# Kernel tuning notes

Hardware: AMD Instinct MI355X
Metric: run time of the kernel (lower is better)

## Reference

```python
import jax, jax.numpy as jnp
import numpy as np

G, T, D = 4, 4096, 2048      # num_groups, tokens_per_group, d_model
E, K, C = 64, 2, 128         # num_experts, num_selected_experts, expert_capacity


def setup_inputs() -> dict:
    key = jax.random.key(0)
    k1, k2 = jax.random.split(key, 2)
    token_inputs = jax.random.normal(k1, (G, T, D), dtype=jnp.float32)
    W = jax.random.normal(k2, (D, E), dtype=jnp.float32) * 0.02  # RouterWeights init std=0.02
    b = jnp.zeros((E,), dtype=jnp.float32)
    return {"token_inputs": token_inputs, "W": W, "b": b,
            "num_experts": E, "expert_capacity": C}


def _route(token_inputs, W, b, num_experts, expert_capacity, k=K, bpr=True):
    # jitter_noise = 0.0 and ignore_padding_tokens = False -> no jitter, no padding mask
    logits = jnp.einsum('gtd,de->gte', token_inputs, W) + b          # [g,t,e]
    probs = jax.nn.softmax(logits, axis=-1)                          # [g,t,e]

    expert_gate, expert_index = jax.lax.top_k(probs, k)              # [g,t,k]

    # Switch Transformer load-balancing loss (eqs 4-6)
    em_lb = jnp.max(jax.nn.one_hot(expert_index, num_experts, dtype=jnp.float32), axis=-2)  # [g,t,e]
    aux_loss = jnp.mean(jnp.mean(em_lb, axis=-2) * jnp.mean(probs, axis=-2)) * num_experts ** 2

    # Batch Prioritized Routing: sort tokens by top-1 gate, descending
    if bpr:
        perm = jnp.argsort(-expert_gate[..., 0], axis=-1)            # [g,t]
        expert_index = jnp.take_along_axis(expert_index, perm[..., None], axis=-2)

    g = token_inputs.shape[0]
    # [g,t,k] -> [g,k,t] -> [g,k*t]: all top-1 choices before top-2 choices
    ei = jnp.transpose(expert_index, (0, 2, 1)).reshape(g, -1)
    em = jax.nn.one_hot(ei, num_experts, dtype=jnp.int32)            # [g,k*t,e]
    # position of each token within its chosen expert's buffer (capacity assignment)
    token_priority = jnp.cumsum(em, axis=1) * em - 1.0               # [g,k*t,e]
    token_priority = token_priority.reshape(g, k, -1, num_experts).transpose(0, 2, 1, 3)
    token_priority = jnp.max(token_priority, axis=2)                 # [g,t,e]

    if bpr:
        inv_perm = jnp.argsort(perm, axis=-1)
        token_priority = jnp.take_along_axis(token_priority, inv_perm[..., None], axis=-2)

    # priority >= expert_capacity or < 0 -> dropped (one_hot gives all zeros)
    dispatch = jax.nn.one_hot(token_priority, expert_capacity, dtype=jnp.float32)  # [g,t,e,c]
    combine = probs[..., None] * dispatch                            # [g,t,e,c]

    z_loss = jnp.mean(jnp.square(jax.nn.log_softmax(logits, axis=-1)))
    return dispatch.astype(jnp.bool_), combine, aux_loss, z_loss


def reference(token_inputs, W, b, num_experts, expert_capacity):
    return _route(token_inputs, W, b, num_experts, expert_capacity)
```

## Files before the change

### kernel.cpp

```cpp
#include <hip/hip_runtime.h>
#include <math.h>

constexpr int Gn = 4;
constexpr int Tn = 4096;
constexpr int Dn = 2048;
constexpr int En = 64;
constexpr int Cn = 128;
constexpr int NT = Gn * Tn;
constexpr size_t NDC = (size_t)NT * En * Cn;


__global__ __launch_bounds__(1024) void k_main(
    const float* __restrict__ x, const float* __restrict__ Wm,
    const float* __restrict__ bias,
    float* __restrict__ gate, int* __restrict__ e1a, int* __restrict__ e2a,
    float* __restrict__ p1a, float* __restrict__ p2a,
    double* __restrict__ spartG, double* __restrict__ zpartArr)
{
    __shared__ float xs[64 * 68];
    __shared__ float ws[64 * 64];
    __shared__ double zrow[64];

    const int tid  = threadIdx.x;
    const int lane = tid & 63;
    const int wave = tid >> 6;
    const int er   = lane & 15;
    const int tr   = lane >> 4;
    const int row  = wave * 4 + tr;
    const int tok0 = blockIdx.x * 64;

    const int sx_row = tid >> 4;
    const int sx_col = tid & 15;

    float acc[4] = {0.f, 0.f, 0.f, 0.f};

    float4 px = *(const float4*)(x + (size_t)(tok0 + sx_row) * Dn + 4 * sx_col);
    float4 pw = ((const float4*)Wm)[tid];

    const float* xsp = xs + row * 68;
    const float* wsp = ws + 4 * er;

    for (int it = 0; it < 32; ++it) {
        *(float4*)(xs + sx_row * 68 + 4 * sx_col) = px;
        ((float4*)ws)[tid] = pw;
        __syncthreads();

        if (it < 31) {
            const int k0 = (it + 1) * 64;
            px = *(const float4*)(x + (size_t)(tok0 + sx_row) * Dn + k0 + 4 * sx_col);
            pw = ((const float4*)(Wm + (size_t)k0 * En))[tid];
        }

        {
        #pragma clang fp contract(off)
        #pragma unroll 4
        for (int kk = 0; kk < 16; ++kk) {
            float4 xq = *(const float4*)(xsp + 4 * kk);
            #pragma unroll
            for (int j = 0; j < 4; ++j) {
                float4 wf = *(const float4*)(wsp + (4 * kk + j) * 64);
                float xv = ((const float*)&xq)[j];
                acc[0] = acc[0] + xv * wf.x;
                acc[1] = acc[1] + xv * wf.y;
                acc[2] = acc[2] + xv * wf.z;
                acc[3] = acc[3] + xv * wf.w;
            }
        }
        }
        __syncthreads();
    }

    {
    #pragma clang fp contract(off)
    #pragma unroll
    for (int j = 0; j < 4; ++j)
        xs[row * 68 + 4 * er + j] = acc[j] + bias[4 * er + j];
    }
    __syncthreads();

    if (tid < 64) {
        const float* lrow = xs + tid * 68;
        float* erow = ws + tid * 64;

        float m = lrow[0];
        for (int i = 1; i < 64; ++i) m = fmaxf(m, lrow[i]);

        for (int i = 0; i < 64; ++i) {
            float d = lrow[i] - m;
            erow[i] = (float)exp((double)d);
        }

        float r8[8];
        #pragma unroll
        for (int j2 = 0; j2 < 8; ++j2) r8[j2] = erow[j2];
        for (int mIt = 1; mIt < 8; ++mIt)
            #pragma unroll
            for (int j2 = 0; j2 < 8; ++j2) r8[j2] += erow[8 * mIt + j2];
        float S = ((r8[0] + r8[1]) + (r8[2] + r8[3]))
                + ((r8[4] + r8[5]) + (r8[6] + r8[7]));

        float av = -1.0f, bv = -1.0f; int ai = 0, bi = 0;
        for (int i = 0; i < 64; ++i) {
            float p = erow[i] / S;
            erow[i] = p;
            if (p > av)      { bv = av; bi = ai; av = p; ai = i; }
            else if (p > bv) { bv = p; bi = i; }
        }

        int tok = tok0 + tid;
        gate[tok] = av;
        e1a[tok] = ai;
        e2a[tok] = bi;
        p1a[tok] = av;
        p2a[tok] = bv;

        double lse = (double)m + log((double)S);
        double zz = 0.0;
        for (int i = 0; i < 64; ++i) {
            double d = (double)lrow[i] - lse;
            zz += d * d;
        }
        zrow[tid] = zz;
    }
    __syncthreads();

    if (tid < 64) {
        double s = 0.0;
        for (int t2 = 0; t2 < 64; ++t2) s += (double)ws[t2 * 64 + tid];
        spartG[blockIdx.x * 64 + tid] = s;
        if (tid == 0) {
            double z = 0.0;
            for (int t2 = 0; t2 < 64; ++t2) z += zrow[t2];
            zpartArr[blockIdx.x] = z;
        }
    }
}

__global__ __launch_bounds__(1024) void k_sortfill(
    const float* __restrict__ gate,
    const int* __restrict__ e1a, const int* __restrict__ e2a,
    int* __restrict__ eseq, int* __restrict__ tseq)
{
    __shared__ float key[4096];
    __shared__ int   val[4096];

    const int g = blockIdx.x;
    for (int i = threadIdx.x; i < Tn; i += 1024) {
        key[i] = gate[g * Tn + i];
        val[i] = i;
    }
    __syncthreads();
    for (int k = 2; k <= Tn; k <<= 1) {
        for (int j = k >> 1; j > 0; j >>= 1) {
            for (int i = threadIdx.x; i < Tn; i += 1024) {
                int ixj = i ^ j;
                if (ixj > i) {
                    bool dir = ((i & k) == 0);
                    float ka = key[i], kb = key[ixj];
                    int   va = val[i], vb = val[ixj];
                    bool bFirst = (kb > ka) || (kb == ka && vb < va);
                    if (bFirst == dir) {
                        key[i] = kb; key[ixj] = ka;
                        val[i] = vb; val[ixj] = va;
                    }
                }
            }
            __syncthreads();
        }
    }
    for (int i = threadIdx.x; i < Tn; i += 1024) {
        int tok = val[i];
        int b = g * 2 * Tn;
        tseq[b + i]      = tok;
        tseq[b + Tn + i] = tok;
        eseq[b + i]      = e1a[g * Tn + tok];
        eseq[b + Tn + i] = e2a[g * Tn + tok];
    }
}

__global__ __launch_bounds__(256) void k_priofill(
    const int* __restrict__ eseq, const int* __restrict__ tseq,
    int* __restrict__ pr1, int* __restrict__ pr2, int* __restrict__ cnt)
{
    if (threadIdx.x >= 64) return;

    const int g = blockIdx.x;
    const int lane = threadIdx.x;
    const int gb = g * 2 * Tn;
    int base = 0;

    int e   = eseq[gb + lane];
    int tok = tseq[gb + lane];

    for (int c = 0; c < 2 * Tn / 64; ++c) {
        int en = 0, tn2 = 0;
        if (c < 2 * Tn / 64 - 1) {
            en  = eseq[gb + (c + 1) * 64 + lane];
            tn2 = tseq[gb + (c + 1) * 64 + lane];
        }

        unsigned long long m  = ~0ull;
        unsigned long long mo = ~0ull;
        #pragma unroll
        for (int bb = 0; bb < 6; ++bb) {
            unsigned long long bal = __ballot((e >> bb) & 1);
            m  &= ((e    >> bb) & 1) ? bal : ~bal;
            mo &= ((lane >> bb) & 1) ? bal : ~bal;
        }
        int rank   = __popcll(m & ((1ull << lane) - 1ull));
        int myBase = __shfl(base, e);
        int pr     = myBase + rank;
        int j      = c * 64 + lane;
        if (j < Tn) pr1[g * Tn + tok] = pr;
        else        pr2[g * Tn + tok] = pr;
        base += __popcll(mo);

        e = en; tok = tn2;
    }
    cnt[g * En + lane] = base;
}

__global__ __launch_bounds__(256) void k_scatfin(
    const int* __restrict__ e1a, const int* __restrict__ e2a,
    const float* __restrict__ p1a, const float* __restrict__ p2a,
    const int* __restrict__ pr1, const int* __restrict__ pr2,
    const int* __restrict__ cnt, const double* __restrict__ spartG,
    const double* __restrict__ zpartArr, float* __restrict__ out)
{
    if (blockIdx.x == 64) {
        __shared__ double red[256];
        __shared__ double zred[256];
        int t = threadIdx.x;
        int g = t >> 6, e = t & 63;
        double s = 0.0;
        #pragma unroll 8
        for (int lb = 0; lb < 64; ++lb)
            s += spartG[((g << 6) + lb) * 64 + e];
        red[t]  = (double)cnt[t] * s;
        zred[t] = zpartArr[t];
        __syncthreads();
        for (int st = 128; st; st >>= 1) {
            if (t < st) { red[t] += red[t + st]; zred[t] += zred[t + st]; }
            __syncthreads();
        }
        if (t == 0) {
            double aux = red[0] * ((double)En / ((double)Gn * (double)Tn * (double)Tn));
            out[2 * NDC]     = (float)aux;
            out[2 * NDC + 1] = (float)(zred[0] / ((double)Gn * Tn * En));
        }
        return;
    }

    int tok = blockIdx.x * 256 + threadIdx.x;
    size_t base = (size_t)tok * En * Cn;
    int p = pr1[tok];
    if (p < Cn) {
        size_t o = base + (size_t)e1a[tok] * Cn + p;
        out[o] = 1.0f;
        out[NDC + o] = p1a[tok];
    }
    p = pr2[tok];
    if (p < Cn) {
        size_t o = base + (size_t)e2a[tok] * Cn + p;
        out[o] = 1.0f;
        out[NDC + o] = p2a[tok];
    }
}

extern "C" void kernel_launch(void* const* d_in, const int* in_sizes, int n_in,
                              void* d_out, int out_size, void* d_ws, size_t ws_size,
                              hipStream_t stream)
{
    const float* x    = (const float*)d_in[0];
    const float* Wm   = (const float*)d_in[1];
    const float* bias = (const float*)d_in[2];
    float* out = (float*)d_out;

    double* spartG   = (double*)d_ws;
    double* zpartArr = spartG + 256 * 64;
    float* gate = (float*)(zpartArr + 256);
    float* p1a  = gate + NT;
    float* p2a  = p1a + NT;
    int* e1a  = (int*)(p2a + NT);
    int* e2a  = e1a + NT;
    int* pr1  = e2a + NT;
    int* pr2  = pr1 + NT;
    int* cnt  = pr2 + NT;
    int* eseq = cnt + Gn * En;
    int* tseq = eseq + Gn * 2 * Tn;

    k_main<<<256, 1024, 0, stream>>>(x, Wm, bias, gate, e1a, e2a,
                                     p1a, p2a, spartG, zpartArr);

    k_sortfill<<<4, 1024, 0, stream>>>(gate, e1a, e2a, eseq, tseq);

    k_priofill<<<4, 256, 0, stream>>>(eseq, tseq, pr1, pr2, cnt);

    k_scatfin<<<65, 256, 0, stream>>>(e1a, e2a, p1a, p2a, pr1, pr2,
                                      cnt, spartG, zpartArr, out);
}
```

Before: 1.151 ms.

## Replace global bitonic sort and serial priority scan with per-expert rank counting

Drops the per-group bitonic sort and the single-wave sequential priority scan. Instead it launches one block per (group, expert) that collects that expert's tokens and computes each token's capacity position by counting higher-gated tokens in the same expert. This moves the work from 4 lightly parallel blocks to 256 blocks. The cost is quadratic in tokens per expert, which is small for balanced routing but could grow with skewed routing.

Result: faster. 1.059 ms (-8.0%).

```diff
diff --git a/kernel.cpp b/kernel.cpp
--- a/kernel.cpp
+++ b/kernel.cpp
@@ -136,88 +136,64 @@
     }
 }
 
-__global__ __launch_bounds__(1024) void k_sortfill(
+__global__ __launch_bounds__(256) void k_rank(
     const float* __restrict__ gate,
     const int* __restrict__ e1a, const int* __restrict__ e2a,
-    int* __restrict__ eseq, int* __restrict__ tseq)
-{
-    __shared__ float key[4096];
-    __shared__ int   val[4096];
-
-    const int g = blockIdx.x;
-    for (int i = threadIdx.x; i < Tn; i += 1024) {
-        key[i] = gate[g * Tn + i];
-        val[i] = i;
-    }
-    __syncthreads();
-    for (int k = 2; k <= Tn; k <<= 1) {
-        for (int j = k >> 1; j > 0; j >>= 1) {
-            for (int i = threadIdx.x; i < Tn; i += 1024) {
-                int ixj = i ^ j;
-                if (ixj > i) {
-                    bool dir = ((i & k) == 0);
-                    float ka = key[i], kb = key[ixj];
-                    int   va = val[i], vb = val[ixj];
-                    bool bFirst = (kb > ka) || (kb == ka && vb < va);
-                    if (bFirst == dir) {
-                        key[i] = kb; key[ixj] = ka;
-                        val[i] = vb; val[ixj] = va;
-                    }
-                }
-            }
-            __syncthreads();
-        }
-    }
-    for (int i = threadIdx.x; i < Tn; i += 1024) {
-        int tok = val[i];
-        int b = g * 2 * Tn;
-        tseq[b + i]      = tok;
-        tseq[b + Tn + i] = tok;
-        eseq[b + i]      = e1a[g * Tn + tok];
-        eseq[b + Tn + i] = e2a[g * Tn + tok];
-    }
-}
-
-__global__ __launch_bounds__(256) void k_priofill(
-    const int* __restrict__ eseq, const int* __restrict__ tseq,
     int* __restrict__ pr1, int* __restrict__ pr2, int* __restrict__ cnt)
 {
-    if (threadIdx.x >= 64) return;
-
-    const int g = blockIdx.x;
-    const int lane = threadIdx.x;
-    const int gb = g * 2 * Tn;
-    int base = 0;
-
-    int e   = eseq[gb + lane];
-    int tok = tseq[gb + lane];
-
-    for (int c = 0; c < 2 * Tn / 64; ++c) {
-        int en = 0, tn2 = 0;
-        if (c < 2 * Tn / 64 - 1) {
-            en  = eseq[gb + (c + 1) * 64 + lane];
-            tn2 = tseq[gb + (c + 1) * 64 + lane];
-        }
-
-        unsigned long long m  = ~0ull;
-        unsigned long long mo = ~0ull;
-        #pragma unroll
-        for (int bb = 0; bb < 6; ++bb) {
-            unsigned long long bal = __ballot((e >> bb) & 1);
-            m  &= ((e    >> bb) & 1) ? bal : ~bal;
-            mo &= ((lane >> bb) & 1) ? bal : ~bal;
-        }
-        int rank   = __popcll(m & ((1ull << lane) - 1ull));
-        int myBase = __shfl(base, e);
-        int pr     = myBase + rank;
-        int j      = c * 64 + lane;
-        if (j < Tn) pr1[g * Tn + tok] = pr;
-        else        pr2[g * Tn + tok] = pr;
-        base += __popcll(mo);
-
-        e = en; tok = tn2;
-    }
-    cnt[g * En + lane] = base;
+    __shared__ int   ltok[4096];
+    __shared__ float lgat[4096];
+    __shared__ int   ncnt;
+
+    const int g = blockIdx.x >> 6;
+    const int e = blockIdx.x & 63;
+    const int tid = threadIdx.x;
+    const int gb = g * Tn;
+
+    if (tid == 0) ncnt = 0;
+    __syncthreads();
+    for (int t = tid; t < Tn; t += 256) {
+        if (e1a[gb + t] == e) {
+            int idx = atomicAdd(&ncnt, 1);
+            ltok[idx] = t;
+            lgat[idx] = gate[gb + t];
+        }
+    }
+    __syncthreads();
+    const int n1 = ncnt;
+    for (int i = tid; i < n1; i += 256) {
+        float gi = lgat[i]; int ti = ltok[i];
+        int r = 0;
+        for (int j = 0; j < n1; ++j) {
+            float gj = lgat[j]; int tj = ltok[j];
+            r += (gj > gi) || (gj == gi && tj < ti);
+        }
+        pr1[gb + ti] = r;
+    }
+    __syncthreads();
+
+    if (tid == 0) ncnt = 0;
+    __syncthreads();
+    for (int t = tid; t < Tn; t += 256) {
+        if (e2a[gb + t] == e) {
+            int idx = atomicAdd(&ncnt, 1);
+            ltok[idx] = t;
+            lgat[idx] = gate[gb + t];
+        }
+    }
+    __syncthreads();
+    const int n2 = ncnt;
+    for (int i = tid; i < n2; i += 256) {
+        float gi = lgat[i]; int ti = ltok[i];
+        int r = 0;
+        for (int j = 0; j < n2; ++j) {
+            float gj = lgat[j]; int tj = ltok[j];
+            r += (gj > gi) || (gj == gi && tj < ti);
+        }
+        pr2[gb + ti] = n1 + r;
+    }
+
+    if (tid == 0) cnt[g * En + e] = n1 + n2;
 }
 
 __global__ __launch_bounds__(256) void k_scatfin(
@@ -286,15 +262,11 @@
     int* pr1  = e2a + NT;
     int* pr2  = pr1 + NT;
     int* cnt  = pr2 + NT;
-    int* eseq = cnt + Gn * En;
-    int* tseq = eseq + Gn * 2 * Tn;
 
     k_main<<<256, 1024, 0, stream>>>(x, Wm, bias, gate, e1a, e2a,
                                      p1a, p2a, spartG, zpartArr);
 
-    k_sortfill<<<4, 1024, 0, stream>>>(gate, e1a, e2a, eseq, tseq);
-
-    k_priofill<<<4, 256, 0, stream>>>(eseq, tseq, pr1, pr2, cnt);
+    k_rank<<<Gn * En, 256, 0, stream>>>(gate, e1a, e2a, pr1, pr2, cnt);
 
     k_scatfin<<<65, 256, 0, stream>>>(e1a, e2a, p1a, p2a, pr1, pr2,
                                       cnt, spartG, zpartArr, out);
```
